# Optimization experiments

Measured on AMD Instinct MI355X. Metric: run time of the kernel, lower is better.

## Reference

```python
import jax, jax.numpy as jnp
import numpy as np

B, T, C, H, D, W = 4, 4096, 1024, 16, 64, 128  # batch, seq, n_embd, n_head, head_dim, window
NB = T // W  # number of query blocks
EPS = 1e-6


def _rms(x, w):
    # RMSNorm over last dim
    return x * jax.lax.rsqrt(jnp.mean(x * x, axis=-1, keepdims=True) + EPS) * w


def _rope(x, pos_ids):
    # MRoPE: pos_ids [T,3]; axis_id maps each freq to one of 3 axes
    inv_freq = 1.0 / (1e6 ** (jnp.arange(0, D, 2, dtype=jnp.float32) / D))  # [D/2]
    axis_id = jnp.arange(D // 2) % 3
    positions = pos_ids[:, axis_id].astype(jnp.float32)  # [T, D/2]
    freqs = positions * inv_freq  # [T, D/2]
    emb = jnp.concatenate([freqs, freqs], axis=-1)  # [T, D]
    cos = jnp.cos(emb)[None, None]  # [1,1,T,D]
    sin = jnp.sin(emb)[None, None]
    x1, x2 = x[..., : D // 2], x[..., D // 2 :]
    rot = jnp.concatenate([-x2, x1], axis=-1)
    return x * cos + rot * sin


def setup_inputs() -> dict:
    key = jax.random.key(0)
    ks = jax.random.split(key, 3)
    x = jax.random.normal(ks[0], (B, T, C), jnp.float32)
    pos = jnp.arange(T, dtype=jnp.int32)
    pos_ids = jnp.stack([pos, pos, pos], axis=-1)  # [T,3] text positions
    w_attn = jax.random.normal(ks[1], (C, C + 2 * D), jnp.float32) * 0.02
    w_proj = jax.random.normal(ks[2], (C, C), jnp.float32) * 0.02
    q_norm_w = jnp.ones((D,), jnp.float32)
    k_norm_w = jnp.ones((D,), jnp.float32)
    return {"x": x, "pos_ids": pos_ids, "w_attn": w_attn, "w_proj": w_proj,
            "q_norm_w": q_norm_w, "k_norm_w": k_norm_w}


def reference(x, pos_ids, w_attn, w_proj, q_norm_w, k_norm_w):
    # fused qkv projection (torch Linear without bias; weight stored [in,out])
    qkv = x @ w_attn  # [B,T,C+2D]
    q = qkv[..., :C].reshape(B, T, H, D).transpose(0, 2, 1, 3)  # [B,H,T,D]
    k = qkv[..., C : C + D][:, None]  # [B,1,T,D] single KV head (MQA)
    v = qkv[..., C + D :][:, None]  # [B,1,T,D]
    q = _rope(_rms(q, q_norm_w), pos_ids)
    k = _rope(_rms(k, k_norm_w), pos_ids)
    # sliding-window attention (q >= kv and q - kv <= W), computed in blocks of W
    qb = q.reshape(B, H, NB, W, D)
    kb = k.reshape(B, NB, W, D)
    vb = v.reshape(B, NB, W, D)
    kp = jnp.concatenate([jnp.zeros_like(kb[:, :1]), kb[:, :-1]], axis=1)  # prev k block
    vp = jnp.concatenate([jnp.zeros_like(vb[:, :1]), vb[:, :-1]], axis=1)
    kv_k = jnp.concatenate([kp, kb], axis=2)  # [B,NB,2W,D]
    kv_v = jnp.concatenate([vp, vb], axis=2)
    n = jnp.arange(NB)[:, None, None]
    qr = jnp.arange(W)[None, :, None]
    kr = jnp.arange(2 * W)[None, None, :]
    q_abs = n * W + qr
    kv_abs = (n - 1) * W + kr
    mask = (q_abs >= kv_abs) & (q_abs - kv_abs <= W) & (kv_abs >= 0)  # [NB,W,2W]
    scores = jnp.einsum("bhnqd,bnkd->bhnqk", qb, kv_k) / jnp.sqrt(jnp.float32(D))
    scores = jnp.where(mask[None, None], scores, -1e30)
    attn = jax.nn.softmax(scores, axis=-1)
    y = jnp.einsum("bhnqk,bnkd->bhnqd", attn, kv_v)  # [B,H,NB,W,D]
    y = y.reshape(B, H, T, D).transpose(0, 2, 1, 3).reshape(B, T, C)
    return y @ w_proj
```

## Files before the change

kernel.cpp:

```cpp
#include <hip/hip_runtime.h>


typedef __attribute__((ext_vector_type(8))) short short8;
typedef __attribute__((ext_vector_type(4))) float f32x4;
typedef __attribute__((ext_vector_type(16))) float f32x16;
typedef __attribute__((ext_vector_type(4))) unsigned uint4v;

#define DEV static __device__ __forceinline__

DEV unsigned short f2bf(float f) {
  unsigned u = __builtin_bit_cast(unsigned, f);
  u += 0x7fffu + ((u >> 16) & 1u);
  return (unsigned short)(u >> 16);
}
DEV float bf2f(unsigned short s) {
  unsigned u = ((unsigned)s) << 16;
  return __builtin_bit_cast(float, u);
}
DEV unsigned cvtpk(float a, float b) {
  unsigned r;
  asm("v_cvt_pk_bf16_f32 %0, %1, %2" : "=v"(r) : "v"(a), "v"(b));
  return r;
}

DEV f32x4 mfma16(short8 a, short8 b, f32x4 c) {
  return __builtin_amdgcn_mfma_f32_16x16x32_bf16(a, b, c, 0, 0, 0);
}
DEV f32x16 mfma32(short8 a, short8 b, f32x16 c) {
  return __builtin_amdgcn_mfma_f32_32x32x16_bf16(a, b, c, 0, 0, 0);
}

DEV void gload16(const void* g, void* l) {
  __builtin_amdgcn_global_load_lds(
      (const __attribute__((address_space(1))) unsigned int*)(unsigned long long)g,
      (__attribute__((address_space(3))) unsigned int*)(unsigned int)(unsigned long long)l,
      16, 0, 0);
}

__global__ __launch_bounds__(256) void k_prep(const float* __restrict__ x,
                                              short* __restrict__ xb,
                                              const float* __restrict__ wa,
                                              short* __restrict__ wabt,
                                              const float* __restrict__ wp,
                                              short* __restrict__ wpbt,
                                              const int* __restrict__ pos,
                                              float* __restrict__ trig) {
  __shared__ float tl[32][33];
  int bid = blockIdx.x, tid = threadIdx.x;
  if (bid < 16384) {
    int i = bid * 256 + tid;
    float4 v = ((const float4*)x)[i];
    short4 o;
    o.x = (short)f2bf(v.x); o.y = (short)f2bf(v.y);
    o.z = (short)f2bf(v.z); o.w = (short)f2bf(v.w);
    ((short4*)xb)[i] = o;
    return;
  }
  if (bid < 16384 + 1152 + 1024) {
    const float* W; short* Wt; int N, local;
    if (bid < 16384 + 1152) { local = bid - 16384; W = wa; Wt = wabt; N = 1152; }
    else { local = bid - 16384 - 1152; W = wp; Wt = wpbt; N = 1024; }
    int k0 = (local & 31) * 32, n0 = (local >> 5) * 32;
    int tx = tid & 31, ty = tid >> 5;
#pragma unroll
    for (int i = 0; i < 4; ++i)
      tl[ty + i * 8][tx] = W[(size_t)(k0 + ty + i * 8) * N + n0 + tx];
    __syncthreads();
#pragma unroll
    for (int i = 0; i < 4; ++i)
      Wt[(size_t)(n0 + ty + i * 8) * 1024 + k0 + tx] = (short)f2bf(tl[tx][ty + i * 8]);
    return;
  }
  {
    int idx = (bid - 16384 - 1152 - 1024) * 256 + tid;
    int t = idx >> 5, j = idx & 31;
    float invf = __expf((float)j * (-13.815510558f / 32.f));
    float p = (float)pos[t * 3 + (j % 3)];
    float s, c;
    sincosf(p * invf, &s, &c);
    ((float2*)trig)[idx] = make_float2(c, s);
  }
}

__global__ __launch_bounds__(256) void k_gemmkv(const short* __restrict__ A,
                                                const short* __restrict__ Bt,
                                                const float* __restrict__ trig,
                                                const float* __restrict__ kw,
                                                short* __restrict__ kb2,
                                                short* __restrict__ vtg) {
  __shared__ short As[128 * 32];
  __shared__ short Bs[128 * 32];
  const int K = 1024;
  int bid = blockIdx.x;
  int bm = (bid & 7) * 16 + (bid >> 3);
  int tid = threadIdx.x, lane = tid & 63, wid = tid >> 6;
  int wr = wid >> 1, wc = wid & 1;
  int lo = lane & 15, hi = lane >> 4;
  const short* Ab = A + (size_t)(bm * 128 + (tid >> 2)) * K + (tid & 3) * 8;
  const short* Bb = Bt + (size_t)(tid >> 2) * K + (tid & 3) * 8;
  f32x4 acc[4][4] = {};
  for (int kt = 0; kt < K; kt += 32) {
    gload16(Ab + kt,            As + tid * 8);
    gload16(Ab + kt + 64 * K,   As + 2048 + tid * 8);
    gload16(Bb + kt,            Bs + tid * 8);
    gload16(Bb + kt + 64 * K,   Bs + 2048 + tid * 8);
    __syncthreads();
    short8 a[4], b[4];
#pragma unroll
    for (int m = 0; m < 4; ++m)
      a[m] = *(const short8*)&As[(wr * 64 + m * 16 + lo) * 32 + hi * 8];
#pragma unroll
    for (int n = 0; n < 4; ++n)
      b[n] = *(const short8*)&Bs[(wc * 64 + n * 16 + lo) * 32 + hi * 8];
#pragma unroll
    for (int m = 0; m < 4; ++m)
#pragma unroll
      for (int n = 0; n < 4; ++n)
        acc[m][n] = mfma16(a[m], b[n], acc[m][n]);
    __syncthreads();
  }
  int tg0 = (bm * 128 + wr * 64) & 4095;
  int bb  = (bm * 128) >> 12;
  if (wc == 0) {
    float w0 = kw[lo], w1 = kw[16 + lo], w2 = kw[32 + lo], w3 = kw[48 + lo];
    const float2* tb = (const float2*)trig;
#pragma unroll
    for (int m = 0; m < 4; ++m)
#pragma unroll
      for (int r = 0; r < 4; ++r) {
        float x0 = acc[m][0][r], x1 = acc[m][1][r];
        float x2 = acc[m][2][r], x3 = acc[m][3][r];
        float ss = x0 * x0 + x1 * x1 + x2 * x2 + x3 * x3;
        ss += __shfl_xor(ss, 1); ss += __shfl_xor(ss, 2);
        ss += __shfl_xor(ss, 4); ss += __shfl_xor(ss, 8);
        float rn = rsqrtf(ss * 0.015625f + 1e-6f);
        x0 *= rn * w0; x1 *= rn * w1; x2 *= rn * w2; x3 *= rn * w3;
        int tp = tg0 + m * 16 + hi * 4 + r;
        float2 cs0 = tb[tp * 32 + lo];
        float2 cs1 = tb[tp * 32 + 16 + lo];
        float o0 = x0 * cs0.x - x2 * cs0.y;
        float o1 = x1 * cs1.x - x3 * cs1.y;
        float o2 = x2 * cs0.x + x0 * cs0.y;
        float o3 = x3 * cs1.x + x1 * cs1.y;
        size_t tb_ = ((size_t)bb * 4096 + tp) * 64;
        kb2[tb_ + lo]      = (short)f2bf(o0);
        kb2[tb_ + 16 + lo] = (short)f2bf(o1);
        kb2[tb_ + 32 + lo] = (short)f2bf(o2);
        kb2[tb_ + 48 + lo] = (short)f2bf(o3);
      }
  } else {
#pragma unroll
    for (int m = 0; m < 4; ++m)
#pragma unroll
      for (int nf = 0; nf < 4; ++nf) {
        int dd = nf * 16 + lo;
        short4 o;
        o.x = (short)f2bf(acc[m][nf][0]);
        o.y = (short)f2bf(acc[m][nf][1]);
        o.z = (short)f2bf(acc[m][nf][2]);
        o.w = (short)f2bf(acc[m][nf][3]);
        *(short4*)&vtg[((size_t)(bb * 64 + dd)) * 4096 + tg0 + m * 16 + hi * 4] = o;
      }
  }
}

__global__ __launch_bounds__(256, 2) void k_gemmbig(
    const short* __restrict__ A, const short* __restrict__ Bt,
    void* __restrict__ Cout, int M, int N, int K, int outBf16,
    const float* __restrict__ trig, const float* __restrict__ qw,
    short* __restrict__ qb2, int mode) {
  __shared__ short sm[24576];
  int nbn = N >> 7;
  int nwg = (M >> 8) * nbn;
  int bid = blockIdx.x;
  int swz = (bid & 7) * (nwg >> 3) + (bid >> 3);
  int bm = swz / nbn, bn = swz % nbn;
  int tid = threadIdx.x, wid = tid >> 6, lane = tid & 63;
  int wm = wid >> 1, wn = wid & 1;
  int lo = lane & 15, hi = lane >> 4;
  int NT = K >> 6;

  int r0 = tid >> 3, ch = tid & 7;
  int sc = ch ^ (r0 & 7);
  const short* aS0 = A  + (size_t)(bm * 256 + r0) * K + sc * 8;
  const short* bS0 = Bt + (size_t)(bn * 128 + r0) * K + sc * 8;

  int aRd[2];
#pragma unroll
  for (int kk = 0; kk < 2; ++kk)
    aRd[kk] = (((kk << 2) | hi) ^ (lo & 7)) * 8;

  short8 Afr[8][2];
  short8 Bfr[4][2];
  f32x4 acc[8][4] = {};

  auto rdA = [&](int m0) {
#pragma unroll
    for (int m = 0; m < 4; ++m)
#pragma unroll
      for (int kk = 0; kk < 2; ++kk)
        Afr[m0 + m][kk] =
            *(const short8*)&sm[(wm * 128 + (m0 + m) * 16 + lo) * 64 + aRd[kk]];
  };
  auto rdB = [&]() {
#pragma unroll
    for (int nf = 0; nf < 4; ++nf)
#pragma unroll
      for (int kk = 0; kk < 2; ++kk)
        Bfr[nf][kk] =
            *(const short8*)&sm[16384 + (wn * 64 + nf * 16 + lo) * 64 + aRd[kk]];
  };
  auto quad = [&](int m0, int n0) {
    __builtin_amdgcn_s_setprio(1);
#pragma unroll
    for (int m = 0; m < 4; ++m)
#pragma unroll
      for (int j = 0; j < 2; ++j)
#pragma unroll
        for (int kk = 0; kk < 2; ++kk)
          acc[m0 + m][n0 + j] = mfma16(Afr[m0 + m][kk], Bfr[n0 + j][kk],
                                       acc[m0 + m][n0 + j]);
    __builtin_amdgcn_s_setprio(0);
  };

  for (int jt = 0; jt < NT; ++jt) {
#pragma unroll
    for (int k = 0; k < 8; ++k)
      gload16(aS0 + jt * 64 + (size_t)32 * k * K, sm + (tid + k * 256) * 8);
#pragma unroll
    for (int k = 0; k < 4; ++k)
      gload16(bS0 + jt * 64 + (size_t)32 * k * K,
              sm + 16384 + (tid + k * 256) * 8);
    __syncthreads();
    rdA(0); rdB(); rdA(4);
    quad(0, 0); quad(0, 2); quad(4, 0); quad(4, 2);
    __syncthreads();
  }

  if (mode == 1) {
    int tg0 = (bm * 256 + wm * 128) & 4095;
    int bb  = (bm * 256) >> 12;
    int hh  = bn * 2 + wn;
    float w0 = qw[lo], w1 = qw[16 + lo], w2 = qw[32 + lo], w3 = qw[48 + lo];
    short* dst = qb2 + (size_t)((bb * 16 + hh) * 4096) * 64;
    const float2* tb = (const float2*)trig;
#pragma unroll
    for (int m = 0; m < 8; ++m)
#pragma unroll
      for (int r = 0; r < 4; ++r) {
        float x0 = acc[m][0][r], x1 = acc[m][1][r];
        float x2 = acc[m][2][r], x3 = acc[m][3][r];
        float ss = x0 * x0 + x1 * x1 + x2 * x2 + x3 * x3;
        ss += __shfl_xor(ss, 1); ss += __shfl_xor(ss, 2);
        ss += __shfl_xor(ss, 4); ss += __shfl_xor(ss, 8);
        float rn = rsqrtf(ss * 0.015625f + 1e-6f);
        x0 *= rn * w0; x1 *= rn * w1; x2 *= rn * w2; x3 *= rn * w3;
        int tp = tg0 + m * 16 + hi * 4 + r;
        float2 cs0 = tb[tp * 32 + lo];
        float2 cs1 = tb[tp * 32 + 16 + lo];
        float o0 = x0 * cs0.x - x2 * cs0.y;
        float o1 = x1 * cs1.x - x3 * cs1.y;
        float o2 = x2 * cs0.x + x0 * cs0.y;
        float o3 = x3 * cs1.x + x1 * cs1.y;
        size_t tb_ = (size_t)tp * 64;
        dst[tb_ + lo]      = (short)f2bf(o0);
        dst[tb_ + 16 + lo] = (short)f2bf(o1);
        dst[tb_ + 32 + lo] = (short)f2bf(o2);
        dst[tb_ + 48 + lo] = (short)f2bf(o3);
      }
    return;
  }

  int row0 = bm * 256 + wm * 128 + hi * 4;
  int col0 = bn * 128 + wn * 64 + lo;
  if (outBf16) {
    short* C = (short*)Cout;
#pragma unroll
    for (int m = 0; m < 8; ++m)
#pragma unroll
      for (int nf = 0; nf < 4; ++nf)
#pragma unroll
        for (int r = 0; r < 4; ++r)
          C[(size_t)(row0 + m * 16 + r) * N + col0 + nf * 16] = (short)f2bf(acc[m][nf][r]);
  } else {
    float* C = (float*)Cout;
#pragma unroll
    for (int m = 0; m < 8; ++m)
#pragma unroll
      for (int nf = 0; nf < 4; ++nf)
#pragma unroll
        for (int r = 0; r < 4; ++r)
          C[(size_t)(row0 + m * 16 + r) * N + col0 + nf * 16] = acc[m][nf][r];
  }
}

__global__ __launch_bounds__(256, 4) void k_attn(const short* __restrict__ qb,
                                                 const short* __restrict__ kb,
                                                 const short* __restrict__ vtg,
                                                 short* __restrict__ y) {
  __shared__ __align__(16) char smem[33792];
  short* ks  = (short*)smem;
  short* vts = (short*)(smem + 16384);
  int bid = blockIdx.x;
  int swz = (bid & 7) * 256 + (bid >> 3);
  int h = swz & 15, n = (swz >> 4) & 31, b = swz >> 9;
  int tid = threadIdx.x, wid = tid >> 6, lane = tid & 63;
  int lo = lane & 31, hi = lane >> 5;

  const short* qrow = qb + (size_t)((b * 16 + h) * 4096 + n * 128 + wid * 32 + lo) * 64;
  short8 aq[4];
#pragma unroll
  for (int s = 0; s < 4; ++s) aq[s] = *(const short8*)(qrow + s * 16 + hi * 8);

  f32x16 O0 = {}, O1 = {};
  float mrun = -1e30f, lrun = 0.f;
  int qr = wid * 32 + lo;
  const float SC = 0.125f * 1.4426950408889634f;

  for (int hf = (n == 0) ? 1 : 0; hf < 2; ++hf) {
    int tg = (n - 1 + hf) * 128;
#pragma unroll
    for (int p = 0; p < 4; ++p) {
      int idx = p * 256 + tid;
      int r = idx >> 3, dc = idx & 7;
      gload16(kb + (size_t)(b * 4096 + tg + r) * 64 + ((dc ^ (r & 7)) << 3),
              ks + idx * 8);
    }
#pragma unroll
    for (int p = 0; p < 4; ++p) {
      int idx = p * 256 + tid;
      int dd = idx >> 4, s = idx & 15;
      gload16(vtg + (size_t)(b * 64 + dd) * 4096 + tg + ((s ^ (dd & 7)) << 3),
              vts + idx * 8);
    }
    __syncthreads();

#pragma unroll
    for (int mt = 0; mt < 4; ++mt) {
      f32x16 S = {};
      int r = mt * 32 + lo;
#pragma unroll
      for (int kst = 0; kst < 4; ++kst) {
        short8 kf = *(const short8*)&ks[r * 64 + ((((kst << 1) | hi) ^ (r & 7)) << 3)];
        S = mfma32(kf, aq[kst], S);
      }
#pragma unroll
      for (int rr = 0; rr < 16; ++rr) {
        int kg = hf * 128 + mt * 32 + (rr & 3) + ((rr >> 2) << 3) + (hi << 2);
        S[rr] = (kg >= qr && kg <= qr + 128) ? S[rr] * SC : -30000.f;
      }
      float pmax = S[0];
#pragma unroll
      for (int rr = 1; rr < 16; ++rr) pmax = fmaxf(pmax, S[rr]);
      pmax = fmaxf(pmax, __shfl_xor(pmax, 32));
      if (!__all(pmax - mrun <= 8.f)) {
        float mn = fmaxf(mrun, pmax);
        float al = exp2f(mrun - mn);
        lrun *= al; mrun = mn;
#pragma unroll
        for (int rr = 0; rr < 16; ++rr) { O0[rr] *= al; O1[rr] *= al; }
      }
      float ls = 0.f;
#pragma unroll
      for (int rr = 0; rr < 16; ++rr) { S[rr] = exp2f(S[rr] - mrun); ls += S[rr]; }
      ls += __shfl_xor(ls, 32);
      lrun += ls;
#pragma unroll
      for (int h2 = 0; h2 < 2; ++h2) {
        int b0 = h2 * 8;
        unsigned pk0 = cvtpk(S[b0 + 0], S[b0 + 1]);
        unsigned pk1 = cvtpk(S[b0 + 2], S[b0 + 3]);
        unsigned pk2 = cvtpk(S[b0 + 4], S[b0 + 5]);
        unsigned pk3 = cvtpk(S[b0 + 6], S[b0 + 7]);
        asm("v_permlane32_swap_b32 %0, %1" : "+v"(pk0), "+v"(pk2));
        asm("v_permlane32_swap_b32 %0, %1" : "+v"(pk1), "+v"(pk3));
        uint4v uw; uw.x = pk0; uw.y = pk1; uw.z = pk2; uw.w = pk3;
        short8 pb = __builtin_bit_cast(short8, uw);
        int kc = mt * 4 + h2 * 2 + hi;
        short8 vb0 = *(const short8*)&vts[lo * 128 + ((kc ^ (lo & 7)) << 3)];
        short8 vb1 = *(const short8*)&vts[(32 + lo) * 128 + ((kc ^ (lo & 7)) << 3)];
        O0 = mfma32(vb0, pb, O0);
        O1 = mfma32(vb1, pb, O1);
      }
    }
    __syncthreads();
  }

  float inv = 1.f / lrun;
  float* ot = (float*)smem + wid * 2112;
#pragma unroll
  for (int r = 0; r < 16; ++r) {
    int d0 = (r & 3) + ((r >> 2) << 3) + (hi << 2);
    ot[d0 * 33 + lo]        = O0[r] * inv;
    ot[(d0 + 32) * 33 + lo] = O1[r] * inv;
  }
  __syncthreads();
  int tok = lane >> 3, dc = lane & 7;
#pragma unroll
  for (int g = 0; g < 4; ++g) {
    int q = g * 8 + tok;
    short8 o8;
#pragma unroll
    for (int jj = 0; jj < 8; ++jj)
      o8[jj] = (short)f2bf(ot[(dc * 8 + jj) * 33 + q]);
    *(short8*)&y[(size_t)(b * 4096 + n * 128 + wid * 32 + q) * 1024 + h * 64 + dc * 8] = o8;
  }
}

extern "C" void kernel_launch(void* const* d_in, const int* in_sizes, int n_in,
                              void* d_out, int out_size, void* d_ws, size_t ws_size,
                              hipStream_t stream) {
  const float* x      = (const float*)d_in[0];
  const int*   pos    = (const int*)d_in[1];
  const float* w_attn = (const float*)d_in[2];
  const float* w_proj = (const float*)d_in[3];
  const float* qw     = (const float*)d_in[4];
  const float* kw     = (const float*)d_in[5];

  char* ws = (char*)d_ws;
  short* xb   = (short*)ws;
  short* wabt = (short*)(ws + 33554432);
  short* wpbt = (short*)(ws + 35913728);
  short* qb2  = (short*)(ws + 38010880);
  short* kb2  = (short*)(ws + 71565312);
  short* vtg  = (short*)(ws + 73662464);
  float* trig = (float*)(ws + 75759616);
  short* ybuf = xb;

  hipLaunchKernelGGL(k_prep, dim3(16384 + 1152 + 1024 + 512), dim3(256), 0, stream,
                     x, xb, w_attn, wabt, w_proj, wpbt, pos, trig);
  hipLaunchKernelGGL(k_gemmkv, dim3(128), dim3(256), 0, stream, xb,
                     wabt + (size_t)1024 * 1024, trig, kw, kb2, vtg);
  hipLaunchKernelGGL(k_gemmbig, dim3(512), dim3(256), 0, stream, xb, wabt,
                     (void*)nullptr, 16384, 1024, 1024, 1, trig, qw, qb2, 1);
  hipLaunchKernelGGL(k_attn, dim3(2048), dim3(256), 0, stream, qb2, kb2, vtg, ybuf);
  hipLaunchKernelGGL(k_gemmbig, dim3(512), dim3(256), 0, stream, ybuf, wpbt, d_out,
                     16384, 1024, 1024, 0,
                     (const float*)nullptr, (const float*)nullptr,
                     (short*)nullptr, 0);
}
```

Before: 160.7 us.

## Switch big GEMM from 16x16x32 to 32x32x16 MFMA tiles

Rewrites the big GEMM's inner loop to use 32x32 MFMA instructions with f32x16 accumulators instead of 16x16 MFMA with f32x4 accumulators. LDS fragment reads are restructured per k-step, and the fused RMSNorm+RoPE epilogue and plain output stores are remapped to the 32x32 accumulator layout. The aim is fewer LDS reads per FLOP and fewer MFMA issues. In exchange, the epilogue reduction needs one more shuffle stage, and fragment loads are no longer batched ahead of the MFMAs.

```diff
diff --git a/kernel.cpp b/kernel.cpp
--- a/kernel.cpp
+++ b/kernel.cpp
@@ -177,7 +177,7 @@
   int bm = swz / nbn, bn = swz % nbn;
   int tid = threadIdx.x, wid = tid >> 6, lane = tid & 63;
   int wm = wid >> 1, wn = wid & 1;
-  int lo = lane & 15, hi = lane >> 4;
+  int col = lane & 31, hi32 = lane >> 5;
   int NT = K >> 6;
 
   int r0 = tid >> 3, ch = tid & 7;
@@ -185,43 +185,7 @@
   const short* aS0 = A  + (size_t)(bm * 256 + r0) * K + sc * 8;
   const short* bS0 = Bt + (size_t)(bn * 128 + r0) * K + sc * 8;
 
-  int aRd[2];
-#pragma unroll
-  for (int kk = 0; kk < 2; ++kk)
-    aRd[kk] = (((kk << 2) | hi) ^ (lo & 7)) * 8;
-
-  short8 Afr[8][2];
-  short8 Bfr[4][2];
-  f32x4 acc[8][4] = {};
-
-  auto rdA = [&](int m0) {
-#pragma unroll
-    for (int m = 0; m < 4; ++m)
-#pragma unroll
-      for (int kk = 0; kk < 2; ++kk)
-        Afr[m0 + m][kk] =
-            *(const short8*)&sm[(wm * 128 + (m0 + m) * 16 + lo) * 64 + aRd[kk]];
-  };
-  auto rdB = [&]() {
-#pragma unroll
-    for (int nf = 0; nf < 4; ++nf)
-#pragma unroll
-      for (int kk = 0; kk < 2; ++kk)
-        Bfr[nf][kk] =
-            *(const short8*)&sm[16384 + (wn * 64 + nf * 16 + lo) * 64 + aRd[kk]];
-  };
-  auto quad = [&](int m0, int n0) {
-    __builtin_amdgcn_s_setprio(1);
-#pragma unroll
-    for (int m = 0; m < 4; ++m)
-#pragma unroll
-      for (int j = 0; j < 2; ++j)
-#pragma unroll
-        for (int kk = 0; kk < 2; ++kk)
-          acc[m0 + m][n0 + j] = mfma16(Afr[m0 + m][kk], Bfr[n0 + j][kk],
-                                       acc[m0 + m][n0 + j]);
-    __builtin_amdgcn_s_setprio(0);
-  };
+  f32x16 acc[4][2] = {};
 
   for (int jt = 0; jt < NT; ++jt) {
 #pragma unroll
@@ -232,8 +196,28 @@
       gload16(bS0 + jt * 64 + (size_t)32 * k * K,
               sm + 16384 + (tid + k * 256) * 8);
     __syncthreads();
-    rdA(0); rdB(); rdA(4);
-    quad(0, 0); quad(0, 2); quad(4, 0); quad(4, 2);
+#pragma unroll
+    for (int kst = 0; kst < 4; ++kst) {
+      int c = (kst << 1) | hi32;
+      short8 af[4], bf[2];
+#pragma unroll
+      for (int mt = 0; mt < 4; ++mt) {
+        int row = wm * 128 + mt * 32 + col;
+        af[mt] = *(const short8*)&sm[row * 64 + ((c ^ (row & 7)) << 3)];
+      }
+#pragma unroll
+      for (int nt = 0; nt < 2; ++nt) {
+        int row = wn * 64 + nt * 32 + col;
+        bf[nt] = *(const short8*)&sm[16384 + row * 64 + ((c ^ (row & 7)) << 3)];
+      }
+      __builtin_amdgcn_s_setprio(1);
+#pragma unroll
+      for (int mt = 0; mt < 4; ++mt)
+#pragma unroll
+        for (int nt = 0; nt < 2; ++nt)
+          acc[mt][nt] = mfma32(af[mt], bf[nt], acc[mt][nt]);
+      __builtin_amdgcn_s_setprio(0);
+    }
     __syncthreads();
   }
 
@@ -241,56 +225,55 @@
     int tg0 = (bm * 256 + wm * 128) & 4095;
     int bb  = (bm * 256) >> 12;
     int hh  = bn * 2 + wn;
-    float w0 = qw[lo], w1 = qw[16 + lo], w2 = qw[32 + lo], w3 = qw[48 + lo];
+    float w0 = qw[col], w1 = qw[32 + col];
     short* dst = qb2 + (size_t)((bb * 16 + hh) * 4096) * 64;
     const float2* tb = (const float2*)trig;
 #pragma unroll
-    for (int m = 0; m < 8; ++m)
-#pragma unroll
-      for (int r = 0; r < 4; ++r) {
-        float x0 = acc[m][0][r], x1 = acc[m][1][r];
-        float x2 = acc[m][2][r], x3 = acc[m][3][r];
-        float ss = x0 * x0 + x1 * x1 + x2 * x2 + x3 * x3;
-        ss += __shfl_xor(ss, 1); ss += __shfl_xor(ss, 2);
-        ss += __shfl_xor(ss, 4); ss += __shfl_xor(ss, 8);
+    for (int mt = 0; mt < 4; ++mt)
+#pragma unroll
+      for (int r = 0; r < 16; ++r) {
+        float x0 = acc[mt][0][r], x1 = acc[mt][1][r];
+        float ss = x0 * x0 + x1 * x1;
+        ss += __shfl_xor(ss, 1);  ss += __shfl_xor(ss, 2);
+        ss += __shfl_xor(ss, 4);  ss += __shfl_xor(ss, 8);
+        ss += __shfl_xor(ss, 16);
         float rn = rsqrtf(ss * 0.015625f + 1e-6f);
-        x0 *= rn * w0; x1 *= rn * w1; x2 *= rn * w2; x3 *= rn * w3;
-        int tp = tg0 + m * 16 + hi * 4 + r;
-        float2 cs0 = tb[tp * 32 + lo];
-        float2 cs1 = tb[tp * 32 + 16 + lo];
-        float o0 = x0 * cs0.x - x2 * cs0.y;
-        float o1 = x1 * cs1.x - x3 * cs1.y;
-        float o2 = x2 * cs0.x + x0 * cs0.y;
-        float o3 = x3 * cs1.x + x1 * cs1.y;
+        x0 *= rn * w0; x1 *= rn * w1;
+        int tp = tg0 + mt * 32 + (r & 3) + ((r >> 2) << 3) + (hi32 << 2);
+        float2 cs = tb[tp * 32 + col];
+        float o0 = x0 * cs.x - x1 * cs.y;
+        float o1 = x1 * cs.x + x0 * cs.y;
         size_t tb_ = (size_t)tp * 64;
-        dst[tb_ + lo]      = (short)f2bf(o0);
-        dst[tb_ + 16 + lo] = (short)f2bf(o1);
-        dst[tb_ + 32 + lo] = (short)f2bf(o2);
-        dst[tb_ + 48 + lo] = (short)f2bf(o3);
+        dst[tb_ + col]      = (short)f2bf(o0);
+        dst[tb_ + 32 + col] = (short)f2bf(o1);
       }
     return;
   }
 
-  int row0 = bm * 256 + wm * 128 + hi * 4;
-  int col0 = bn * 128 + wn * 64 + lo;
+  int row0 = bm * 256 + wm * 128;
+  int col0 = bn * 128 + wn * 64;
   if (outBf16) {
     short* C = (short*)Cout;
 #pragma unroll
-    for (int m = 0; m < 8; ++m)
-#pragma unroll
-      for (int nf = 0; nf < 4; ++nf)
-#pragma unroll
-        for (int r = 0; r < 4; ++r)
-          C[(size_t)(row0 + m * 16 + r) * N + col0 + nf * 16] = (short)f2bf(acc[m][nf][r]);
+    for (int mt = 0; mt < 4; ++mt)
+#pragma unroll
+      for (int nt = 0; nt < 2; ++nt)
+#pragma unroll
+        for (int r = 0; r < 16; ++r) {
+          int row = row0 + mt * 32 + (r & 3) + ((r >> 2) << 3) + (hi32 << 2);
+          C[(size_t)row * N + col0 + nt * 32 + col] = (short)f2bf(acc[mt][nt][r]);
+        }
   } else {
     float* C = (float*)Cout;
 #pragma unroll
-    for (int m = 0; m < 8; ++m)
-#pragma unroll
-      for (int nf = 0; nf < 4; ++nf)
-#pragma unroll
-        for (int r = 0; r < 4; ++r)
-          C[(size_t)(row0 + m * 16 + r) * N + col0 + nf * 16] = acc[m][nf][r];
+    for (int mt = 0; mt < 4; ++mt)
+#pragma unroll
+      for (int nt = 0; nt < 2; ++nt)
+#pragma unroll
+        for (int r = 0; r < 16; ++r) {
+          int row = row0 + mt * 32 + (r & 3) + ((r >> 2) << 3) + (hi32 << 2);
+          C[(size_t)row * N + col0 + nt * 32 + col] = acc[mt][nt][r];
+        }
   }
 }
 
```

After: 173.2 us. +7.7%, slower.
